# Kernel tuning notes

Measured on AMD Instinct MI355X. Metric: run time of the kernel, lower is better.

Reference implementation:

```python
import jax, jax.numpy as jnp
import numpy as np

# Module hyperparameters (from init_kwargs)
B, KP, H = 64, 21, 256          # batch, keypoints, heatmap size
KS, SIGMA = 9, 1.5              # Gaussian kernel size / sigma
PAD = KS // 2


def _gaussian_kernel2d(ksize, sigma):
    # matches cv2.getGaussianKernel(ksize, sigma) @ its transpose
    xs = np.arange(ksize, dtype=np.float64) - (ksize - 1) / 2.0
    g = np.exp(-(xs ** 2) / (2.0 * sigma ** 2))
    g /= g.sum()
    return (np.outer(g, g)).astype(np.float32)


def setup_inputs() -> dict:
    key = jax.random.key(0)
    # integer pixel coordinates (row, col) in [0, H)
    x = jax.random.randint(key, (B, KP, 2), 0, H, dtype=jnp.int32)
    kernel2d = jnp.asarray(_gaussian_kernel2d(KS, SIGMA))
    return {"x": x, "kernel2d": kernel2d}


def reference(x, kernel2d):
    # scatter: bg[b, k, crd0, crd1] = 10  (one point per (b, k), no duplicates)
    crd = x.reshape(-1, 2)                       # [B*KP, 2]
    flat = jnp.arange(B * KP)
    b_idx, k_idx = flat // KP, flat % KP
    bg = jnp.zeros((B, KP, H, H), jnp.float32)
    bg = bg.at[b_idx, k_idx, crd[:, 0], crd[:, 1]].set(10.0)

    # block-diagonal conv == depthwise conv with the shared Gaussian patch
    w = jnp.broadcast_to(kernel2d[None, None], (KP, 1, KS, KS))
    out = jax.lax.conv_general_dilated(
        bg, w,
        window_strides=(1, 1),
        padding=[(PAD, PAD), (PAD, PAD)],
        dimension_numbers=("NCHW", "OIHW", "NCHW"),
        feature_group_count=KP,
    )
    return out
```

## Files before the change

kernel.cpp:

```cpp
#include <hip/hip_runtime.h>

#define BB   64
#define KP   21
#define HH   256
#define KS   9
#define PADK 4

#define NPLANES       (BB * KP)
#define F4_PER_PLANE  (HH * HH / 4)
#define NBLOCKS       2048
#define THREADS       256
#define F4_TOTAL      (NPLANES * F4_PER_PLANE)
#define F4_PER_BLOCK  (F4_TOTAL / NBLOCKS)
#define F4_PER_THREAD (F4_PER_BLOCK / THREADS)

typedef float vfloat4 __attribute__((ext_vector_type(4)));

__global__ __launch_bounds__(THREADS)
void heatmap_persist_kernel(const int* __restrict__ x,
                            const float* __restrict__ k2d,
                            vfloat4* __restrict__ out) {
    const int t  = threadIdx.x;
    const int b0 = blockIdx.x * F4_PER_BLOCK;

    vfloat4* ptr = out + b0 + t;
#pragma unroll
    for (int ch = 0; ch < F4_PER_THREAD; ++ch) {
        *ptr = (vfloat4)0.0f;
        ptr += THREADS;
    }

    __syncthreads();

    const int p_lo = b0 / F4_PER_PLANE;
    const int p_hi = (b0 + F4_PER_BLOCK - 1) / F4_PER_PLANE;

    if (t < KS * KS) {
        const int dy = t / KS;
        const int dx = t - dy * KS;
        for (int p = p_lo; p <= p_hi; ++p) {
            const int r = x[2 * p];
            const int c = x[2 * p + 1];
            const int i = r - PADK + dy;
            const int j = c - PADK + dx;
            if (i < 0 || i >= HH || j < 0 || j >= HH) continue;
            const int g4 = p * F4_PER_PLANE + i * (HH / 4) + (j >> 2);
            if (g4 < b0 || g4 >= b0 + F4_PER_BLOCK) continue;
            const float v = 10.0f * k2d[(KS - 1 - dy) * KS + (KS - 1 - dx)];
            ((float*)out)[(size_t)g4 * 4 + (j & 3)] = v;
        }
    }
}

extern "C" void kernel_launch(void* const* d_in, const int* in_sizes, int n_in,
                              void* d_out, int out_size, void* d_ws, size_t ws_size,
                              hipStream_t stream) {
    const int*   x   = (const int*)d_in[0];
    const float* k2d = (const float*)d_in[1];
    vfloat4*     out = (vfloat4*)d_out;

    heatmap_persist_kernel<<<NBLOCKS, THREADS, 0, stream>>>(x, k2d, out);
}
```

Baseline: 68.10 us.

## Zero output with grid-strided sweeps and remap Gaussian stamping per block

The zero fill changes from each block owning a contiguous chunk to a grid-wide strided sweep, so every iteration writes one fully contiguous region across all blocks. Stamping is remapped to match: each block owns a 4-row band of a fixed plane residue class (plane mod 32) and writes only the Gaussian entries that fall in its rows. The aim is better DRAM write locality during the dominant zero fill. The cost is that each active thread now loops over 42 planes and reads their coordinates instead of touching one or two planes.

```diff
diff --git a/kernel.cpp b/kernel.cpp
--- a/kernel.cpp
+++ b/kernel.cpp
@@ -10,44 +10,43 @@
 #define F4_PER_PLANE  (HH * HH / 4)
 #define NBLOCKS       2048
 #define THREADS       256
+#define NTH_TOTAL     (NBLOCKS * THREADS)
 #define F4_TOTAL      (NPLANES * F4_PER_PLANE)
-#define F4_PER_BLOCK  (F4_TOTAL / NBLOCKS)
-#define F4_PER_THREAD (F4_PER_BLOCK / THREADS)
+#define NSWEEP        (F4_TOTAL / NTH_TOTAL)
 
 typedef float vfloat4 __attribute__((ext_vector_type(4)));
 
 __global__ __launch_bounds__(THREADS)
-void heatmap_persist_kernel(const int* __restrict__ x,
-                            const float* __restrict__ k2d,
-                            vfloat4* __restrict__ out) {
-    const int t  = threadIdx.x;
-    const int b0 = blockIdx.x * F4_PER_BLOCK;
+void heatmap_sweep_kernel(const int* __restrict__ x,
+                          const float* __restrict__ k2d,
+                          vfloat4* __restrict__ out) {
+    const int t = threadIdx.x;
+    const int b = blockIdx.x;
 
-    vfloat4* ptr = out + b0 + t;
+    vfloat4* ptr = out + (b * THREADS + t);
 #pragma unroll
-    for (int ch = 0; ch < F4_PER_THREAD; ++ch) {
+    for (int it = 0; it < NSWEEP; ++it) {
         *ptr = (vfloat4)0.0f;
-        ptr += THREADS;
+        ptr += NTH_TOTAL;
     }
 
     __syncthreads();
 
-    const int p_lo = b0 / F4_PER_PLANE;
-    const int p_hi = (b0 + F4_PER_BLOCK - 1) / F4_PER_PLANE;
-
     if (t < KS * KS) {
-        const int dy = t / KS;
-        const int dx = t - dy * KS;
-        for (int p = p_lo; p <= p_hi; ++p) {
-            const int r = x[2 * p];
-            const int c = x[2 * p + 1];
+        const int dy  = t / KS;
+        const int dx  = t - dy * KS;
+        const int w   = b >> 6;
+        const int rlo = (b & 63) * 4;
+        const float wt = 10.0f * k2d[(KS - 1 - dy) * KS + (KS - 1 - dx)];
+        for (int m = 0; m < NPLANES / 32; ++m) {
+            const int pl = w + (m << 5);
+            const int r = x[2 * pl];
+            const int c = x[2 * pl + 1];
             const int i = r - PADK + dy;
             const int j = c - PADK + dx;
-            if (i < 0 || i >= HH || j < 0 || j >= HH) continue;
-            const int g4 = p * F4_PER_PLANE + i * (HH / 4) + (j >> 2);
-            if (g4 < b0 || g4 >= b0 + F4_PER_BLOCK) continue;
-            const float v = 10.0f * k2d[(KS - 1 - dy) * KS + (KS - 1 - dx)];
-            ((float*)out)[(size_t)g4 * 4 + (j & 3)] = v;
+            if (i >= rlo && i < rlo + 4 && j >= 0 && j < HH) {
+                ((float*)out)[(size_t)pl * (HH * HH) + i * HH + j] = wt;
+            }
         }
     }
 }
@@ -59,5 +58,5 @@
     const float* k2d = (const float*)d_in[1];
     vfloat4*     out = (vfloat4*)d_out;
 
-    heatmap_persist_kernel<<<NBLOCKS, THREADS, 0, stream>>>(x, k2d, out);
+    heatmap_sweep_kernel<<<NBLOCKS, THREADS, 0, stream>>>(x, k2d, out);
 }
```

New measurement: 84.33 us. +23.8%, slower.
